# Optimization experiments

Hardware: AMD Instinct MI355X
Metric: run time of the kernel (lower is better)

Reference implementation:

```python
import jax, jax.numpy as jnp
import numpy as np

NUM_POINTS = 200000
VIEW_NUM = 1
SCALE = 0.05
BIN_RES = 0.01
NUM_BINS = 512
T0 = 0.0
DECAY = 2.0


def setup_inputs() -> dict:
    key = jax.random.key(0)
    k = jax.random.split(key, 6)
    means = jax.random.normal(k[0], (NUM_POINTS, 3), dtype=jnp.float32)
    scan_point = jax.random.normal(k[1], (3,), dtype=jnp.float32)
    # learned params, initialized as in __init__ plus small noise for non-degenerate grads
    colours = 0.01 * jnp.ones((NUM_POINTS, 1), jnp.float32) + 0.001 * jax.random.normal(k[2], (NUM_POINTS, 1), jnp.float32)
    coefficients = 0.1 * jax.random.normal(k[3], (NUM_POINTS, 1), dtype=jnp.float32)
    opacities = 0.1 * jnp.ones((NUM_POINTS, VIEW_NUM), jnp.float32) + 0.01 * jax.random.normal(k[4], (NUM_POINTS, VIEW_NUM), jnp.float32)
    scales = jnp.float32(np.log(SCALE)) * jnp.ones((NUM_POINTS, 1), jnp.float32) + 0.1 * jax.random.normal(k[5], (NUM_POINTS, 1), jnp.float32)
    return {"means": means, "scan_point": scan_point, "colours": colours,
            "coefficients": coefficients, "opacities": opacities, "scales": scales,
            "view_id": 0}


def reference(means, scan_point, colours, coefficients, opacities, scales, view_id):
    # render_conf_hist2: confocal time-of-flight histogram, no rasterization
    intensity = (opacities[:, view_id] ** 2) * (colours[:, 0] ** 2)          # [N]
    coeff = jax.nn.sigmoid(coefficients)                                     # [N,1]
    r0 = jnp.linalg.norm(means - scan_point[None, :], axis=1, keepdims=True) # [N,1]
    r_ = T0 / 2 + (BIN_RES / 2) * jnp.arange(1, NUM_BINS + 1, dtype=jnp.float32)  # [B]
    r = r_[None, :]                                                          # [1,B]
    sigma = jnp.maximum(jnp.mean(jnp.exp(scales), axis=1, keepdims=True), BIN_RES / 2)  # [N,1]
    diff = r - r0                                                            # [N,B]
    e = jnp.exp(-0.5 * (diff / sigma) ** 2)                                  # [N,B]
    pdf1 = np.sqrt(0.5 / np.pi) * e / sigma
    pdf2 = diff * e / (sigma * sigma)
    pdf = coeff * pdf1 + (1.0 - coeff) * pdf2
    pr = jnp.clip(pdf * (BIN_RES / 2), 0.0, 1.0)
    hist = jnp.sum(intensity[:, None] * pr, axis=0)                          # [B]
    return hist / jnp.power(r_, DECAY)
```

## Files before the change

kernel.cpp:

```cpp
#include <hip/hip_runtime.h>
#include <hip/hip_bf16.h>
#include <math.h>


#define NBINS 512
#define TPB 512
#define NBLK 256
#define K_SQRT_HALF_PI 0.3989422804014327f
#define LOG2E 1.4426950408889634f

__device__ __forceinline__ float fast_exp2(float x) {
#if __has_builtin(__builtin_amdgcn_exp2f)
    return __builtin_amdgcn_exp2f(x);
#else
    return exp2f(x);
#endif
}

__global__ __launch_bounds__(TPB) void gauss_scatter(
    const float* __restrict__ means,
    const float* __restrict__ scan_point,
    const float* __restrict__ colours,
    const float* __restrict__ coeffs,
    const float* __restrict__ opac,
    const float* __restrict__ scales,
    const int* __restrict__ view_id,
    float* __restrict__ out,
    int n)
{
    __shared__ float hist[NBINS];
    const int t = threadIdx.x;
    hist[t] = 0.f;
    __syncthreads();

    const int vid = view_id[0];
    const float sx = scan_point[0], sy = scan_point[1], sz = scan_point[2];

    for (int p = blockIdx.x * TPB + t; p < n; p += NBLK * TPB) {
        float dx = means[3 * p + 0] - sx;
        float dy = means[3 * p + 1] - sy;
        float dz = means[3 * p + 2] - sz;
        float r0 = sqrtf(fmaf(dx, dx, fmaf(dy, dy, dz * dz)));
        float sg = fmaxf(expf(scales[p]), 0.005f);
        float inv_s = 1.0f / sg;
        float coeff = 1.0f / (1.0f + expf(-coeffs[p]));
        float op  = opac[p + vid];
        float col = colours[p];
        float ia  = (op * op) * (col * col) * 0.005f;
        float nalpha = 0.5f * LOG2E * inv_s * inv_s;
        float aw = ia * coeff * K_SQRT_HALF_PI * inv_s;
        float bw = ia * (1.0f - coeff) * inv_s * inv_s;

        float rlo = r0 - aw / bw;
        float rhi = fmaf(8.0f, sg, r0);
        int lo = (int)floorf(rlo * 200.f) - 1;
        int hi = (int)floorf(rhi * 200.f);
        lo = lo < 0 ? 0 : lo;
        hi = hi > NBINS - 1 ? NBINS - 1 : hi;
        if (lo > hi) continue;

        float diff0 = fmaf(0.005f, (float)(lo + 1), -r0);
        float e = fast_exp2(-(nalpha * diff0) * diff0);
        float d = fast_exp2(-nalpha * fmaf(0.01f, diff0, 2.5e-5f));
        const float c = fast_exp2(-nalpha * 5.0e-5f);
        float w = fmaf(bw, diff0, aw);
        const float bwd = bw * 0.005f;
        for (int b = lo; b <= hi; ++b) {
            atomicAdd(&hist[b], __saturatef(e * w));
            e *= d;
            d *= c;
            w += bwd;
        }
    }
    __syncthreads();

    const int bin = (t + (blockIdx.x << 4)) & (NBINS - 1);
    float h = hist[bin];
    if (h != 0.f) {
        float r = 0.005f * (float)(bin + 1);
        atomicAdd(&out[bin], h / (r * r));
    }
}

extern "C" void kernel_launch(void* const* d_in, const int* in_sizes, int n_in,
                              void* d_out, int out_size, void* d_ws, size_t ws_size,
                              hipStream_t stream) {
    const float* means = (const float*)d_in[0];
    const float* scan  = (const float*)d_in[1];
    const float* col   = (const float*)d_in[2];
    const float* cf    = (const float*)d_in[3];
    const float* op    = (const float*)d_in[4];
    const float* sc    = (const float*)d_in[5];
    const int*   vid   = (const int*)d_in[6];
    float* out = (float*)d_out;

    const int n = in_sizes[2];
    hipMemsetAsync(d_out, 0, (size_t)out_size * sizeof(float), stream);
    gauss_scatter<<<NBLK, TPB, 0, stream>>>(means, scan, col, cf, op, sc, vid, out, n);
}
```

Before: 87.40 us.

## Distribute each point's bin range across wavefront lanes via readlane broadcast

Each wavefront now loads 64 points, computes their parameters per lane, then loops over the 64 points, broadcasting each point's parameters with readlane so the lanes split that point's bin range. Previously one thread walked its own bins serially, which caused divergence and long per-thread loops. Block size doubles to 1024 so the grid covers all points in a single pass. Each bin now costs a direct exp2 in place of the old recurrence multiplies. Neighbouring lanes hit different bins, which avoids same-address LDS atomic conflicts within a wave, but short ranges leave most lanes idle.

```diff
diff --git a/kernel.cpp b/kernel.cpp
--- a/kernel.cpp
+++ b/kernel.cpp
@@ -1,10 +1,9 @@
 #include <hip/hip_runtime.h>
-#include <hip/hip_bf16.h>
 #include <math.h>
 
 
 #define NBINS 512
-#define TPB 512
+#define TPB 1024
 #define NBLK 256
 #define K_SQRT_HALF_PI 0.3989422804014327f
 #define LOG2E 1.4426950408889634f
@@ -15,6 +14,17 @@
 #else
     return exp2f(x);
 #endif
+}
+
+__device__ __forceinline__ int rdlane_i(int v, int l) {
+#if __has_builtin(__builtin_amdgcn_readlane)
+    return __builtin_amdgcn_readlane(v, l);
+#else
+    return __shfl(v, l, 64);
+#endif
+}
+__device__ __forceinline__ float rdlane_f(float v, int l) {
+    return __int_as_float(rdlane_i(__float_as_int(v), l));
 }
 
 __global__ __launch_bounds__(TPB) void gauss_scatter(
@@ -30,55 +40,74 @@
 {
     __shared__ float hist[NBINS];
     const int t = threadIdx.x;
-    hist[t] = 0.f;
+    if (t < NBINS) hist[t] = 0.f;
     __syncthreads();
 
     const int vid = view_id[0];
     const float sx = scan_point[0], sy = scan_point[1], sz = scan_point[2];
 
-    for (int p = blockIdx.x * TPB + t; p < n; p += NBLK * TPB) {
-        float dx = means[3 * p + 0] - sx;
-        float dy = means[3 * p + 1] - sy;
-        float dz = means[3 * p + 2] - sz;
-        float r0 = sqrtf(fmaf(dx, dx, fmaf(dy, dy, dz * dz)));
-        float sg = fmaxf(expf(scales[p]), 0.005f);
-        float inv_s = 1.0f / sg;
-        float coeff = 1.0f / (1.0f + expf(-coeffs[p]));
-        float op  = opac[p + vid];
-        float col = colours[p];
-        float ia  = (op * op) * (col * col) * 0.005f;
-        float nalpha = 0.5f * LOG2E * inv_s * inv_s;
-        float aw = ia * coeff * K_SQRT_HALF_PI * inv_s;
-        float bw = ia * (1.0f - coeff) * inv_s * inv_s;
+    const int lane = t & 63;
+    const int wid  = t >> 6;
+    const int chunk   = wid * NBLK + blockIdx.x;
+    const int nchunks = (n + 63) >> 6;
 
-        float rlo = r0 - aw / bw;
-        float rhi = fmaf(8.0f, sg, r0);
-        int lo = (int)floorf(rlo * 200.f) - 1;
-        int hi = (int)floorf(rhi * 200.f);
-        lo = lo < 0 ? 0 : lo;
-        hi = hi > NBINS - 1 ? NBINS - 1 : hi;
-        if (lo > hi) continue;
+    float r0 = 0.f, nna = 0.f, aw = 0.f, bw = 0.f;
+    int lo = 0, num = 0;
+    if (chunk < nchunks) {
+        const int p = (chunk << 6) + lane;
+        if (p < n) {
+            float dx = means[3 * p + 0] - sx;
+            float dy = means[3 * p + 1] - sy;
+            float dz = means[3 * p + 2] - sz;
+            r0 = sqrtf(fmaf(dx, dx, fmaf(dy, dy, dz * dz)));
+            float sg = fmaxf(expf(scales[p]), 0.005f);
+            float inv_s = 1.0f / sg;
+            float coeff = 1.0f / (1.0f + expf(-coeffs[p]));
+            float op  = opac[p + vid];
+            float col = colours[p];
+            float ia  = (op * op) * (col * col) * 0.005f;
+            nna = -0.5f * LOG2E * inv_s * inv_s;
+            aw  = ia * coeff * K_SQRT_HALF_PI * inv_s;
+            bw  = ia * (1.0f - coeff) * inv_s * inv_s;
+            float rlo = r0 - aw / bw;
+            float rhi = fmaf(8.0f, sg, r0);
+            int l = (int)floorf(rlo * 200.f) - 1;
+            int h = (int)floorf(rhi * 200.f);
+            l = l < 0 ? 0 : l;
+            h = h > NBINS - 1 ? NBINS - 1 : h;
+            lo  = l;
+            num = (h >= l) ? (h - l + 1) : 0;
+        }
+    }
 
-        float diff0 = fmaf(0.005f, (float)(lo + 1), -r0);
-        float e = fast_exp2(-(nalpha * diff0) * diff0);
-        float d = fast_exp2(-nalpha * fmaf(0.01f, diff0, 2.5e-5f));
-        const float c = fast_exp2(-nalpha * 5.0e-5f);
-        float w = fmaf(bw, diff0, aw);
-        const float bwd = bw * 0.005f;
-        for (int b = lo; b <= hi; ++b) {
+    for (int k = 0; k < 64; ++k) {
+        const int num_k = rdlane_i(num, k);
+        if (num_k <= 0) continue;
+        const int   lo_k  = rdlane_i(lo, k);
+        const float r0_k  = rdlane_f(r0, k);
+        const float nna_k = rdlane_f(nna, k);
+        const float aw_k  = rdlane_f(aw, k);
+        const float bw_k  = rdlane_f(bw, k);
+
+        int b = lo_k + lane;
+        const int bend = lo_k + num_k;
+        float rb = 0.005f * (float)(b + 1);
+        for (; b < bend; b += 64, rb += 0.32f) {
+            float diff = rb - r0_k;
+            float e = fast_exp2((nna_k * diff) * diff);
+            float w = fmaf(bw_k, diff, aw_k);
             atomicAdd(&hist[b], __saturatef(e * w));
-            e *= d;
-            d *= c;
-            w += bwd;
         }
     }
     __syncthreads();
 
-    const int bin = (t + (blockIdx.x << 4)) & (NBINS - 1);
-    float h = hist[bin];
-    if (h != 0.f) {
-        float r = 0.005f * (float)(bin + 1);
-        atomicAdd(&out[bin], h / (r * r));
+    if (t < NBINS) {
+        const int bin = (t + (blockIdx.x << 4)) & (NBINS - 1);
+        float h = hist[bin];
+        if (h != 0.f) {
+            float r = 0.005f * (float)(bin + 1);
+            atomicAdd(&out[bin], h / (r * r));
+        }
     }
 }
 
```

After: 83.81 us. 4.1% less time.
